# Kernel optimization log

Hardware: AMD Instinct MI355X
Metric: run time of the kernel (lower is better)

The kernel has to match this reference:

```python
import jax, jax.numpy as jnp
import numpy as np

B, N, E = 4, 4096, 1024
F_IN, F_OUT, F_EDGE = 128, 128, 64


def setup_inputs() -> dict:
    key = jax.random.key(0)
    k1, k2, k3, k4, k5, k6 = jax.random.split(key, 6)
    node = jax.random.normal(k1, (B, N, F_IN), dtype=jnp.float32)
    edge = jax.random.normal(k2, (B, E, F_EDGE), dtype=jnp.float32)
    # symmetric 0/1 adjacency (sparse-ish, avg degree ~ 2*0.005*N)
    a = (jax.random.uniform(k3, (B, N, N)) < 0.005).astype(jnp.float32)
    node_adj = jnp.maximum(a, jnp.swapaxes(a, 1, 2))
    # D: positive diagonal degree matrix [B,N,N]
    deg = node_adj.sum(-1) + 1.0                      # [B,N], strictly > 0
    D = deg[:, :, None] * jnp.eye(N, dtype=jnp.float32)
    # T: node-edge incidence-like 0/1 matrix [B,N,E]
    T = (jax.random.uniform(k4, (B, N, E)) < 0.002).astype(jnp.float32)
    stdv_n = 1.0 / np.sqrt(F_OUT)
    node_weight = jax.random.uniform(k5, (F_IN, F_OUT), minval=-stdv_n, maxval=stdv_n, dtype=jnp.float32)
    stdv_e = 1.0 / np.sqrt(F_EDGE)
    edge_weight = jax.random.uniform(k6, (F_EDGE,), minval=-stdv_e, maxval=stdv_e, dtype=jnp.float32)
    return {"node": node, "edge": edge, "node_adj": node_adj, "D": D, "T": T,
            "edge_weight": edge_weight, "node_weight": node_weight}


def reference(node, edge, node_adj, D, T, edge_weight, node_weight):
    # D <- sqrt(D); nonzero entries inverted (i.e. D^{-1/2}, zeros stay zero)
    nz = D != 0
    Dinv = jnp.where(nz, 1.0 / jnp.sqrt(jnp.where(nz, D, 1.0)), 0.0)
    # node_adj += I  (first bmm(D, node_adj) in the source is dead code)
    A = node_adj + jnp.eye(node_adj.shape[2], dtype=node_adj.dtype)
    A_tilde = jnp.matmul(A, Dinv)                      # [B,N,N]
    # HePe = edge @ edge_weight -> per-edge scalar; T diag(HePe) T^T fused:
    HePe = jnp.einsum('bef,f->be', edge, edge_weight)  # [B,E]
    S = jnp.einsum('bne,be,bme->bnm', T, HePe, T)      # (T*v) @ T^T, [B,N,N]
    out = jnp.matmul(S * A_tilde, node)                # [B,N,F_IN]
    out = jnp.matmul(out, node_weight)                 # [B,N,F_OUT]
    return out
```

## Files before the change

### kernel.cpp

```cpp
#include <hip/hip_runtime.h>

#define BB 4
#define NN 4096
#define EE 1024
#define FIN 128
#define FE 64
#define CAP 33
#define LSTRIDE 34
#define ESTRIDE 32

#define MI_HEPE (BB * EE / 4)
#define MI_DINV (BB * NN / 256)
#define MI_EFILL 64

typedef unsigned short u16;
typedef unsigned int u32;
typedef unsigned long long u64;

__global__ __launch_bounds__(256) void k_misc(const float* __restrict__ edge,
                                              const float* __restrict__ ew,
                                              const float* __restrict__ D,
                                              float* __restrict__ hepe,
                                              int* __restrict__ ecnt,
                                              float* __restrict__ dinv,
                                              u16* __restrict__ elists) {
    int t = threadIdx.x, lane = t & 63, wid = t >> 6;
    int bid = blockIdx.x;
    if (bid < MI_HEPE) {
        int row = bid * 4 + wid;
        float v = edge[(size_t)row * FE + lane] * ew[lane];
#pragma unroll
        for (int d = 32; d >= 1; d >>= 1) v += __shfl_xor(v, d, 64);
        if (lane == 0) { hepe[row] = v; ecnt[row] = 0; }
    } else if (bid < MI_HEPE + MI_DINV) {
        int idx = (bid - MI_HEPE) * 256 + t;
        int b = idx >> 12, n = idx & (NN - 1);
        float v = D[((size_t)b * NN + n) * NN + n];
        dinv[idx] = (v != 0.f) ? (1.f / sqrtf(v)) : 0.f;
    } else {
        int idx = (bid - MI_HEPE - MI_DINV) * 256 + t;
        uint4* e4 = (uint4*)elists;
        e4[idx] = make_uint4(0xFFFFFFFFu, 0xFFFFFFFFu, 0xFFFFFFFFu, 0xFFFFFFFFu);
    }
}

__global__ __launch_bounds__(256) void k_stage(const float* __restrict__ T,
                                               const float* __restrict__ node,
                                               const float* __restrict__ W,
                                               u16* __restrict__ lists,
                                               int* __restrict__ ecnt,
                                               u16* __restrict__ elists,
                                               float* __restrict__ nodeW,
                                               int gemmBlocks) {
    __shared__ float tile[32][FIN];
    int t = threadIdx.x, lane = t & 63, wid = t >> 6;
    int bid = blockIdx.x;

    if (bid < gemmBlocks) {
        size_t row0 = (size_t)bid * 32;
        const float* sbase = node + row0 * FIN;
        float* dbase = nodeW + row0 * FIN;
#pragma unroll
        for (int k = 0; k < 16; k++) {
            int idx = k * 256 + t;
            tile[idx >> 7][idx & 127] = sbase[idx];
        }
        __syncthreads();
        int f = t & 127, h = t >> 7;
        float acc[16];
#pragma unroll
        for (int j = 0; j < 16; j++) acc[j] = 0.f;
        for (int k = 0; k < 128; k += 2) {
            float w0 = W[k * 128 + f];
            float w1 = W[(k + 1) * 128 + f];
#pragma unroll
            for (int j = 0; j < 16; j++) {
                float2 tv = *(const float2*)&tile[h * 16 + j][k];
                acc[j] += tv.x * w0 + tv.y * w1;
            }
        }
#pragma unroll
        for (int j = 0; j < 16; j++) dbase[(size_t)(h * 16 + j) * 128 + f] = acc[j];
    } else {
        int row = (bid - gemmBlocks) * 4 + wid;
        int b = row >> 12, n = row & (NN - 1);
        const float4* rowT = (const float4*)(T + (size_t)row * EE);
        float4 t0 = rowT[lane], t1 = rowT[64 + lane], t2 = rowT[128 + lane], t3 = rowT[192 + lane];
        float vs[16] = {t0.x, t0.y, t0.z, t0.w, t1.x, t1.y, t1.z, t1.w,
                        t2.x, t2.y, t2.z, t2.w, t3.x, t3.y, t3.z, t3.w};
        int c = 0;
#pragma unroll
        for (int k = 0; k < 16; k++) c += (vs[k] != 0.f);
        int x = c;
#pragma unroll
        for (int d = 1; d < 64; d <<= 1) {
            int o = __shfl_up(x, d, 64);
            if (lane >= d) x += o;
        }
        int tot = __shfl(x, 63, 64);
        int pos = x - c;
        u16* L = lists + (size_t)row * LSTRIDE;
        if (c > 0) {
#pragma unroll
            for (int k = 0; k < 16; k++) {
                if (vs[k] != 0.f) {
                    if (pos < CAP) {
                        int e = ((k >> 2) * 64 + lane) * 4 + (k & 3);
                        L[1 + pos] = (u16)e;
                        int eb = (b << 10) + e;
                        int p2 = atomicAdd(&ecnt[eb], 1);
                        if (p2 < ESTRIDE) elists[(size_t)eb * ESTRIDE + p2] = (u16)n;
                    }
                    pos++;
                }
            }
        }
        if (lane == 0) L[0] = (u16)(tot < CAP ? tot : CAP);
    }
}

__global__ __launch_bounds__(256) void k_gemm(const float* __restrict__ src,
                                              const float* __restrict__ W,
                                              float* __restrict__ dst) {
    __shared__ float tile[32][FIN];
    int t = threadIdx.x;
    size_t row0 = (size_t)blockIdx.x * 32;
    const float* sbase = src + row0 * FIN;
    float* dbase = dst + row0 * FIN;
#pragma unroll
    for (int k = 0; k < 16; k++) {
        int idx = k * 256 + t;
        tile[idx >> 7][idx & 127] = sbase[idx];
    }
    __syncthreads();
    int f = t & 127, h = t >> 7;
    float acc[16];
#pragma unroll
    for (int j = 0; j < 16; j++) acc[j] = 0.f;
    for (int k = 0; k < 128; k += 2) {
        float w0 = W[k * 128 + f];
        float w1 = W[(k + 1) * 128 + f];
#pragma unroll
        for (int j = 0; j < 16; j++) {
            float2 tv = *(const float2*)&tile[h * 16 + j][k];
            acc[j] += tv.x * w0 + tv.y * w1;
        }
    }
#pragma unroll
    for (int j = 0; j < 16; j++) dbase[(size_t)(h * 16 + j) * 128 + f] = acc[j];
}

__global__ __launch_bounds__(256) void k_main(const float* __restrict__ A,
                                              const float* __restrict__ rows,
                                              const float* __restrict__ hepe,
                                              const float* __restrict__ dinv,
                                              const u16* __restrict__ lists,
                                              const u16* __restrict__ elists,
                                              float* __restrict__ out) {
    __shared__ u32   sEB[4][33];
    __shared__ float sH[4][33];
    int t = threadIdx.x, lane = t & 63, wid = t >> 6;
    int row = blockIdx.x * 4 + wid;
    int b = row >> 12, n = row & (NN - 1);
    const u16* L = lists + (size_t)row * LSTRIDE;

    const float2* rows2 = (const float2*)rows;
    float  dn    = dinv[row];
    float  adiag = A[((size_t)b << 24) + ((size_t)n << 12) + n];
    float2 nvd   = rows2[(size_t)row * 64 + lane];

    int cn = L[0];
    int eRaw = 0;
    if (lane <= 32) eRaw = L[1 + lane];
    int eb = (b << 10) + (eRaw & (EE - 1));
    float h = (lane < cn) ? hepe[eb] : 0.f;
    if (lane < cn) {
        sEB[wid][lane] = (u32)eb * ESTRIDE;
        sH[wid][lane]  = h;
    }

    float sd = h;
#pragma unroll
    for (int d = 32; d >= 1; d >>= 1) sd += __shfl_xor(sd, d, 64);

    float cdiag = sd * (adiag + 1.f) * dn;
    float2 acc = make_float2(cdiag * nvd.x, cdiag * nvd.y);

    int P = cn << 5;
    for (int base = 0; base < P; base += 64) {
        int p = base + lane;
        float cc = 0.f; int m = 0;
        if (p < P) {
            int j = p >> 5;
            m = elists[sEB[wid][j] + (p & (ESTRIDE - 1))];
            if (m < NN && m != n) {
                float a = A[((size_t)b << 24) + ((size_t)n << 12) + m];
                if (a != 0.f) cc = sH[wid][j] * a * dinv[(b << 12) + m];
            }
        }
        u64 mask = __ballot(cc != 0.f);
        while (mask) {
            int src = __ffsll(mask) - 1;
            mask &= mask - 1;
            float cb = __shfl(cc, src, 64);
            int   mb = __shfl(m, src, 64);
            float2 nv = rows2[((size_t)((b << 12) + mb)) * 64 + lane];
            acc.x += cb * nv.x;
            acc.y += cb * nv.y;
        }
    }
    float2* out2 = (float2*)out;
    out2[(size_t)row * 64 + lane] = acc;
}

extern "C" void kernel_launch(void* const* d_in, const int* in_sizes, int n_in,
                              void* d_out, int out_size, void* d_ws, size_t ws_size,
                              hipStream_t stream) {
    const float* node     = (const float*)d_in[0];
    const float* edge     = (const float*)d_in[1];
    const float* node_adj = (const float*)d_in[2];
    const float* D        = (const float*)d_in[3];
    const float* T        = (const float*)d_in[4];
    const float* ew       = (const float*)d_in[5];
    const float* W        = (const float*)d_in[6];
    float* out = (float*)d_out;

    char* ws = (char*)d_ws;
    float* hepe  = (float*)ws;                          ws += BB * EE * 4;
    float* dinv  = (float*)ws;                          ws += BB * NN * 4;
    int*   ecnt  = (int*)ws;                            ws += BB * EE * 4;
    u16*   lists = (u16*)ws;                            ws += BB * NN * LSTRIDE * 2;
    u16*   elists= (u16*)ws;                            ws += BB * EE * ESTRIDE * 2;
    size_t small_need = (size_t)(ws - (char*)d_ws);
    float* nodeW = (float*)ws;
    bool fuse = ws_size >= small_need + (size_t)BB * NN * FIN * 4;

    int gemmBlocks = fuse ? (BB * NN / 32) : 0;

    k_misc <<<MI_HEPE + MI_DINV + MI_EFILL, 256, 0, stream>>>(edge, ew, D, hepe,
                                                              ecnt, dinv, elists);
    k_stage<<<gemmBlocks + BB * NN / 4,     256, 0, stream>>>(T, node, W, lists, ecnt,
                                                              elists, nodeW, gemmBlocks);

    if (fuse) {
        k_main<<<BB * NN / 4, 256, 0, stream>>>(node_adj, nodeW, hepe, dinv,
                                                lists, elists, out);
    } else {
        k_main<<<BB * NN / 4, 256, 0, stream>>>(node_adj, node, hepe, dinv,
                                                lists, elists, out);
        k_gemm<<<BB * NN / 32, 256, 0, stream>>>(out, W, out);
    }
}
```

Baseline: 46.58 us.

## Fuse node-weight projection into the sparse aggregation kernel epilogue

Drops the separate node@W GEMM pre-pass (and its fallback post-pass), so the sparse aggregation gathers raw node rows. Each wave then stages its accumulated row in shared memory and multiplies it by W directly before writing the output. This removes the nodeW buffer write and read and the GEMM blocks in the staging kernel. In exchange, every output row redoes a 128x128 matvec with W read from cache per wave, which is less efficient than a tiled GEMM.

```diff
diff --git a/kernel.cpp b/kernel.cpp
--- a/kernel.cpp
+++ b/kernel.cpp
@@ -45,113 +45,49 @@
 }
 
 __global__ __launch_bounds__(256) void k_stage(const float* __restrict__ T,
-                                               const float* __restrict__ node,
-                                               const float* __restrict__ W,
                                                u16* __restrict__ lists,
                                                int* __restrict__ ecnt,
-                                               u16* __restrict__ elists,
-                                               float* __restrict__ nodeW,
-                                               int gemmBlocks) {
-    __shared__ float tile[32][FIN];
+                                               u16* __restrict__ elists) {
     int t = threadIdx.x, lane = t & 63, wid = t >> 6;
-    int bid = blockIdx.x;
-
-    if (bid < gemmBlocks) {
-        size_t row0 = (size_t)bid * 32;
-        const float* sbase = node + row0 * FIN;
-        float* dbase = nodeW + row0 * FIN;
+    int row = blockIdx.x * 4 + wid;
+    int b = row >> 12, n = row & (NN - 1);
+    const float4* rowT = (const float4*)(T + (size_t)row * EE);
+    float4 t0 = rowT[lane], t1 = rowT[64 + lane], t2 = rowT[128 + lane], t3 = rowT[192 + lane];
+    float vs[16] = {t0.x, t0.y, t0.z, t0.w, t1.x, t1.y, t1.z, t1.w,
+                    t2.x, t2.y, t2.z, t2.w, t3.x, t3.y, t3.z, t3.w};
+    int c = 0;
+#pragma unroll
+    for (int k = 0; k < 16; k++) c += (vs[k] != 0.f);
+    int x = c;
+#pragma unroll
+    for (int d = 1; d < 64; d <<= 1) {
+        int o = __shfl_up(x, d, 64);
+        if (lane >= d) x += o;
+    }
+    int tot = __shfl(x, 63, 64);
+    int pos = x - c;
+    u16* L = lists + (size_t)row * LSTRIDE;
+    if (c > 0) {
 #pragma unroll
         for (int k = 0; k < 16; k++) {
-            int idx = k * 256 + t;
-            tile[idx >> 7][idx & 127] = sbase[idx];
-        }
-        __syncthreads();
-        int f = t & 127, h = t >> 7;
-        float acc[16];
-#pragma unroll
-        for (int j = 0; j < 16; j++) acc[j] = 0.f;
-        for (int k = 0; k < 128; k += 2) {
-            float w0 = W[k * 128 + f];
-            float w1 = W[(k + 1) * 128 + f];
-#pragma unroll
-            for (int j = 0; j < 16; j++) {
-                float2 tv = *(const float2*)&tile[h * 16 + j][k];
-                acc[j] += tv.x * w0 + tv.y * w1;
+            if (vs[k] != 0.f) {
+                if (pos < CAP) {
+                    int e = ((k >> 2) * 64 + lane) * 4 + (k & 3);
+                    L[1 + pos] = (u16)e;
+                    int eb = (b << 10) + e;
+                    int p2 = atomicAdd(&ecnt[eb], 1);
+                    if (p2 < ESTRIDE) elists[(size_t)eb * ESTRIDE + p2] = (u16)n;
+                }
+                pos++;
             }
         }
-#pragma unroll
-        for (int j = 0; j < 16; j++) dbase[(size_t)(h * 16 + j) * 128 + f] = acc[j];
-    } else {
-        int row = (bid - gemmBlocks) * 4 + wid;
-        int b = row >> 12, n = row & (NN - 1);
-        const float4* rowT = (const float4*)(T + (size_t)row * EE);
-        float4 t0 = rowT[lane], t1 = rowT[64 + lane], t2 = rowT[128 + lane], t3 = rowT[192 + lane];
-        float vs[16] = {t0.x, t0.y, t0.z, t0.w, t1.x, t1.y, t1.z, t1.w,
-                        t2.x, t2.y, t2.z, t2.w, t3.x, t3.y, t3.z, t3.w};
-        int c = 0;
-#pragma unroll
-        for (int k = 0; k < 16; k++) c += (vs[k] != 0.f);
-        int x = c;
-#pragma unroll
-        for (int d = 1; d < 64; d <<= 1) {
-            int o = __shfl_up(x, d, 64);
-            if (lane >= d) x += o;
-        }
-        int tot = __shfl(x, 63, 64);
-        int pos = x - c;
-        u16* L = lists + (size_t)row * LSTRIDE;
-        if (c > 0) {
-#pragma unroll
-            for (int k = 0; k < 16; k++) {
-                if (vs[k] != 0.f) {
-                    if (pos < CAP) {
-                        int e = ((k >> 2) * 64 + lane) * 4 + (k & 3);
-                        L[1 + pos] = (u16)e;
-                        int eb = (b << 10) + e;
-                        int p2 = atomicAdd(&ecnt[eb], 1);
-                        if (p2 < ESTRIDE) elists[(size_t)eb * ESTRIDE + p2] = (u16)n;
-                    }
-                    pos++;
-                }
-            }
-        }
-        if (lane == 0) L[0] = (u16)(tot < CAP ? tot : CAP);
     }
-}
-
-__global__ __launch_bounds__(256) void k_gemm(const float* __restrict__ src,
-                                              const float* __restrict__ W,
-                                              float* __restrict__ dst) {
-    __shared__ float tile[32][FIN];
-    int t = threadIdx.x;
-    size_t row0 = (size_t)blockIdx.x * 32;
-    const float* sbase = src + row0 * FIN;
-    float* dbase = dst + row0 * FIN;
-#pragma unroll
-    for (int k = 0; k < 16; k++) {
-        int idx = k * 256 + t;
-        tile[idx >> 7][idx & 127] = sbase[idx];
-    }
-    __syncthreads();
-    int f = t & 127, h = t >> 7;
-    float acc[16];
-#pragma unroll
-    for (int j = 0; j < 16; j++) acc[j] = 0.f;
-    for (int k = 0; k < 128; k += 2) {
-        float w0 = W[k * 128 + f];
-        float w1 = W[(k + 1) * 128 + f];
-#pragma unroll
-        for (int j = 0; j < 16; j++) {
-            float2 tv = *(const float2*)&tile[h * 16 + j][k];
-            acc[j] += tv.x * w0 + tv.y * w1;
-        }
-    }
-#pragma unroll
-    for (int j = 0; j < 16; j++) dbase[(size_t)(h * 16 + j) * 128 + f] = acc[j];
+    if (lane == 0) L[0] = (u16)(tot < CAP ? tot : CAP);
 }
 
 __global__ __launch_bounds__(256) void k_main(const float* __restrict__ A,
-                                              const float* __restrict__ rows,
+                                              const float* __restrict__ node,
+                                              const float* __restrict__ W,
                                               const float* __restrict__ hepe,
                                               const float* __restrict__ dinv,
                                               const u16* __restrict__ lists,
@@ -159,12 +95,13 @@
                                               float* __restrict__ out) {
     __shared__ u32   sEB[4][33];
     __shared__ float sH[4][33];
+    __shared__ float sROW[4][FIN];
     int t = threadIdx.x, lane = t & 63, wid = t >> 6;
     int row = blockIdx.x * 4 + wid;
     int b = row >> 12, n = row & (NN - 1);
     const u16* L = lists + (size_t)row * LSTRIDE;
 
-    const float2* rows2 = (const float2*)rows;
+    const float2* rows2 = (const float2*)node;
     float  dn    = dinv[row];
     float  adiag = A[((size_t)b << 24) + ((size_t)n << 12) + n];
     float2 nvd   = rows2[(size_t)row * 64 + lane];
@@ -209,8 +146,20 @@
             acc.y += cb * nv.y;
         }
     }
+
+    sROW[wid][2 * lane]     = acc.x;
+    sROW[wid][2 * lane + 1] = acc.y;
+    float2 o = make_float2(0.f, 0.f);
+    const float2* W2 = (const float2*)W;
+#pragma unroll 4
+    for (int k = 0; k < FIN; k++) {
+        float r = sROW[wid][k];
+        float2 w2 = W2[(size_t)k * 64 + lane];
+        o.x += r * w2.x;
+        o.y += r * w2.y;
+    }
     float2* out2 = (float2*)out;
-    out2[(size_t)row * 64 + lane] = acc;
+    out2[(size_t)row * 64 + lane] = o;
 }
 
 extern "C" void kernel_launch(void* const* d_in, const int* in_sizes, int n_in,
@@ -230,24 +179,11 @@
     float* dinv  = (float*)ws;                          ws += BB * NN * 4;
     int*   ecnt  = (int*)ws;                            ws += BB * EE * 4;
     u16*   lists = (u16*)ws;                            ws += BB * NN * LSTRIDE * 2;
-    u16*   elists= (u16*)ws;                            ws += BB * EE * ESTRIDE * 2;
-    size_t small_need = (size_t)(ws - (char*)d_ws);
-    float* nodeW = (float*)ws;
-    bool fuse = ws_size >= small_need + (size_t)BB * NN * FIN * 4;
-
-    int gemmBlocks = fuse ? (BB * NN / 32) : 0;
+    u16*   elists= (u16*)ws;
 
     k_misc <<<MI_HEPE + MI_DINV + MI_EFILL, 256, 0, stream>>>(edge, ew, D, hepe,
                                                               ecnt, dinv, elists);
-    k_stage<<<gemmBlocks + BB * NN / 4,     256, 0, stream>>>(T, node, W, lists, ecnt,
-                                                              elists, nodeW, gemmBlocks);
-
-    if (fuse) {
-        k_main<<<BB * NN / 4, 256, 0, stream>>>(node_adj, nodeW, hepe, dinv,
-                                                lists, elists, out);
-    } else {
-        k_main<<<BB * NN / 4, 256, 0, stream>>>(node_adj, node, hepe, dinv,
-                                                lists, elists, out);
-        k_gemm<<<BB * NN / 32, 256, 0, stream>>>(out, W, out);
-    }
+    k_stage<<<BB * NN / 4,                  256, 0, stream>>>(T, lists, ecnt, elists);
+    k_main <<<BB * NN / 4,                  256, 0, stream>>>(node_adj, node, W, hepe,
+                                                              dinv, lists, elists, out);
 }
```

After: 90.14 us. 1.94x slower.
